# Performance work log

Hardware: AMD Instinct MI355X
Metric: run time of the kernel (lower is better)

## Reference

```python
import jax, jax.numpy as jnp
import numpy as np

TAU = 0.02  # softmax temperature (logits are divided by tau)


def setup_inputs() -> dict:
    key = jax.random.key(0)
    k1, k2 = jax.random.split(key)
    B, N, H, W = 4, 256, 256, 256
    H_img, W_img = 512, 512
    logits = jax.random.normal(k1, (B, N, H, W), dtype=jnp.float32)
    # ground-truth match coordinates (x, y) in image-pixel space
    gt_xy = jax.random.uniform(k2, (B, N, 2), dtype=jnp.float32) * jnp.array(
        [W_img - 1, H_img - 1], dtype=jnp.float32
    )
    # grid buffer: (H*W, 2) rows of (x, y), x fastest (meshgrid ij, stacked [xs, ys])
    ys, xs = jnp.meshgrid(jnp.arange(H), jnp.arange(W), indexing="ij")
    grid = jnp.stack([xs, ys], axis=-1).reshape(-1, 2).astype(jnp.float32)
    return {"logits": logits, "gt_xy": gt_xy, "grid": grid, "H_img": H_img, "W_img": W_img}


def reference(logits, gt_xy, grid, H_img, W_img):
    B, N, H, W = logits.shape
    # scale gt coords from image pixels to feature-map pixels (per-axis (new-1)/(old-1))
    scale_in = jnp.array([(W - 1) / (W_img - 1), (H - 1) / (H_img - 1)], dtype=logits.dtype)
    gt_fm = gt_xy * scale_in  # (B, N, 2)
    # temperature softmax over flattened spatial dim
    prob = jax.nn.softmax(logits.reshape(B, N, H * W) / TAU, axis=-1)  # (B, N, HW)
    # soft-argmax: expected (x, y) coordinate
    pred = jnp.einsum("bnl,lc->bnc", prob, grid)  # (B, N, 2)
    norm_scale = jnp.array([W - 1, H - 1], dtype=pred.dtype)
    pred_norm = 2.0 * pred / norm_scale - 1.0
    gt_norm = 2.0 * gt_fm / norm_scale - 1.0
    err = jnp.linalg.norm(pred_norm - gt_norm, axis=-1)  # (B, N)
    return err.sum()
```

## Files before the change

kernel.cpp:

```cpp
#include <hip/hip_runtime.h>
#include <math.h>

#define TAU_INV 50.0f

__device__ __forceinline__ void osm_merge(float& m, float& s, float& sx, float& sy,
                                          float m2, float s2, float sx2, float sy2) {
    float nm = fmaxf(m, m2);
    float c1 = __expf(m - nm);
    float c2 = __expf(m2 - nm);
    s  = s  * c1 + s2  * c2;
    sx = sx * c1 + sx2 * c2;
    sy = sy * c1 + sy2 * c2;
    m  = nm;
}

__device__ __forceinline__ void osm_elem(float& m, float& s, float& sx, float& sy,
                                         float a, float fx, float fy) {
    float nm = fmaxf(m, a);
    float c  = __expf(m - nm);
    float w  = __expf(a - nm);
    s  = fmaf(s,  c, w);
    sx = fmaf(sx, c, w * fx);
    sy = fmaf(sy, c, w * fy);
    m  = nm;
}

__global__ __launch_bounds__(256) void soft_argmax_part(
        const float* __restrict__ logits,
        float4* __restrict__ part,
        int W, int elems_per_blk, float invW) {
    const int blk = blockIdx.x;
    const int tid = threadIdx.x;
    const int nvec = elems_per_blk >> 2;
    const float4* b4 = (const float4*)logits + (size_t)blk * (size_t)nvec;
    const int base_l = (blk & 1) * elems_per_blk;

    float m = -INFINITY, s = 0.f, sx = 0.f, sy = 0.f;

    for (int i = tid; i < nvec; i += 512) {
        const int i1 = i + 256;
        float4 v0 = b4[i];
        float4 v1;
        bool have1 = (i1 < nvec);
        if (have1) v1 = b4[i1];

        {
            int l0 = base_l + (i << 2);
            int y0 = (int)((float)l0 * invW);
            if (y0 * W > l0) --y0;
            else if ((y0 + 1) * W <= l0) ++y0;
            int x0 = l0 - y0 * W;
            float fy = (float)y0;
            osm_elem(m, s, sx, sy, v0.x * TAU_INV, (float)(x0 + 0), fy);
            osm_elem(m, s, sx, sy, v0.y * TAU_INV, (float)(x0 + 1), fy);
            osm_elem(m, s, sx, sy, v0.z * TAU_INV, (float)(x0 + 2), fy);
            osm_elem(m, s, sx, sy, v0.w * TAU_INV, (float)(x0 + 3), fy);
        }
        if (have1) {
            int l0 = base_l + (i1 << 2);
            int y0 = (int)((float)l0 * invW);
            if (y0 * W > l0) --y0;
            else if ((y0 + 1) * W <= l0) ++y0;
            int x0 = l0 - y0 * W;
            float fy = (float)y0;
            osm_elem(m, s, sx, sy, v1.x * TAU_INV, (float)(x0 + 0), fy);
            osm_elem(m, s, sx, sy, v1.y * TAU_INV, (float)(x0 + 1), fy);
            osm_elem(m, s, sx, sy, v1.z * TAU_INV, (float)(x0 + 2), fy);
            osm_elem(m, s, sx, sy, v1.w * TAU_INV, (float)(x0 + 3), fy);
        }
    }

    #pragma unroll
    for (int off = 32; off >= 1; off >>= 1) {
        float m2  = __shfl_xor(m,  off);
        float s2  = __shfl_xor(s,  off);
        float sx2 = __shfl_xor(sx, off);
        float sy2 = __shfl_xor(sy, off);
        osm_merge(m, s, sx, sy, m2, s2, sx2, sy2);
    }

    __shared__ float sm[4], ss[4], ssx[4], ssy[4];
    const int wave = tid >> 6, lane = tid & 63;
    if (lane == 0) { sm[wave] = m; ss[wave] = s; ssx[wave] = sx; ssy[wave] = sy; }
    __syncthreads();

    if (tid == 0) {
        #pragma unroll
        for (int wv = 1; wv < 4; ++wv)
            osm_merge(m, s, sx, sy, sm[wv], ss[wv], ssx[wv], ssy[wv]);
        part[blk] = make_float4(m, s, sx, sy);
    }
}

__global__ __launch_bounds__(256) void finish(
        const float4* __restrict__ part,
        const float* __restrict__ gt_xy,
        const int* __restrict__ HimgP,
        const int* __restrict__ WimgP,
        float* __restrict__ out,
        int W, int H, int BN) {
    const int tid = threadIdx.x;
    const float Wimg = (float)WimgP[0];
    const float Himg = (float)HimgP[0];
    const float sxin = (float)(W - 1) / (Wimg - 1.f);
    const float syin = (float)(H - 1) / (Himg - 1.f);
    const float nx = 2.f / (float)(W - 1);
    const float ny = 2.f / (float)(H - 1);

    float acc = 0.f;
    for (int r = tid; r < BN; r += 256) {
        float4 p0 = part[2 * r + 0];
        float4 p1 = part[2 * r + 1];
        float m = p0.x, s = p0.y, sx = p0.z, sy = p0.w;
        osm_merge(m, s, sx, sy, p1.x, p1.y, p1.z, p1.w);
        float px = sx / s;
        float py = sy / s;
        float gx = gt_xy[2 * r + 0] * sxin;
        float gy = gt_xy[2 * r + 1] * syin;
        float dx = (px - gx) * nx;
        float dy = (py - gy) * ny;
        acc += sqrtf(dx * dx + dy * dy);
    }
    #pragma unroll
    for (int off = 32; off >= 1; off >>= 1) acc += __shfl_xor(acc, off);
    __shared__ float sw[4];
    const int wave = tid >> 6, lane = tid & 63;
    if (lane == 0) sw[wave] = acc;
    __syncthreads();
    if (tid == 0) out[0] = sw[0] + sw[1] + sw[2] + sw[3];
}

extern "C" void kernel_launch(void* const* d_in, const int* in_sizes, int n_in,
                              void* d_out, int out_size, void* d_ws, size_t ws_size,
                              hipStream_t stream) {
    const float* logits = (const float*)d_in[0];
    const float* gt_xy  = (const float*)d_in[1];
    const int*   HimgP  = (const int*)d_in[3];
    const int*   WimgP  = (const int*)d_in[4];

    const int HW = in_sizes[2] / 2;
    const int BN = in_sizes[1] / 2;
    int W = 1;
    while (W * W < HW) W <<= 1;
    if (W * W != HW) W = (int)(sqrtf((float)HW) + 0.5f);
    const int H = HW / W;

    float4* part = (float4*)d_ws;
    float*  out  = (float*)d_out;

    const int elems_per_blk = HW / 2;
    soft_argmax_part<<<2 * BN, 256, 0, stream>>>(logits, part, W, elems_per_blk,
                                                 1.0f / (float)W);
    finish<<<1, 256, 0, stream>>>(part, gt_xy, HimgP, WimgP, out, W, H, BN);
}
```

Measured before the change: 51.90 us.

## Fuse finish into soft-argmax kernel, vectorize online softmax per float4 with exp2

The separate finish kernel is folded into the main kernel through a last-block-done atomic counter, which removes one kernel launch. The per-element online softmax now works per float4: it takes a local max of four values, does four exp2 calls plus one merge, and computes x/y coordinates with shifts and masks. The inner loop is unrolled to four float4 loads per iteration to raise memory-level parallelism. The counter lives in the workspace, is never reset, and relies on modulo of gridDim. W is also assumed to be a power of two, and the non-square fallback was removed.

Result: slower. 105.3 us (+102.9%).

```diff
diff --git a/kernel.cpp b/kernel.cpp
--- a/kernel.cpp
+++ b/kernel.cpp
@@ -2,132 +2,142 @@
 #include <math.h>
 
 #define TAU_INV 50.0f
+#define LOG2E   1.4426950408889634f
 
-__device__ __forceinline__ void osm_merge(float& m, float& s, float& sx, float& sy,
-                                          float m2, float s2, float sx2, float sy2) {
-    float nm = fmaxf(m, m2);
-    float c1 = __expf(m - nm);
-    float c2 = __expf(m2 - nm);
-    s  = s  * c1 + s2  * c2;
-    sx = sx * c1 + sx2 * c2;
-    sy = sy * c1 + sy2 * c2;
-    m  = nm;
+#if __has_builtin(__builtin_amdgcn_exp2f)
+#define EXP2(x) __builtin_amdgcn_exp2f(x)
+#else
+#define EXP2(x) __expf((x) * 0.6931471805599453f)
+#endif
+
+struct Quad { float m, s, sx, sy; };
+
+__device__ __forceinline__ Quad qmerge(const Quad a, const Quad b) {
+    Quad r;
+    r.m = fmaxf(a.m, b.m);
+    float ca = EXP2(a.m - r.m);
+    float cb = EXP2(b.m - r.m);
+    r.s  = fmaf(a.s,  ca, b.s  * cb);
+    r.sx = fmaf(a.sx, ca, b.sx * cb);
+    r.sy = fmaf(a.sy, ca, b.sy * cb);
+    return r;
 }
 
-__device__ __forceinline__ void osm_elem(float& m, float& s, float& sx, float& sy,
-                                         float a, float fx, float fy) {
-    float nm = fmaxf(m, a);
-    float c  = __expf(m - nm);
-    float w  = __expf(a - nm);
-    s  = fmaf(s,  c, w);
-    sx = fmaf(sx, c, w * fx);
-    sy = fmaf(sy, c, w * fy);
-    m  = nm;
+__device__ __forceinline__ Quad quad_of(const float4 v, const float x0, const float fy) {
+    const float k = TAU_INV * LOG2E;
+    float a0 = v.x * k, a1 = v.y * k, a2 = v.z * k, a3 = v.w * k;
+    float m4 = fmaxf(fmaxf(a0, a1), fmaxf(a2, a3));
+    float w0 = EXP2(a0 - m4), w1 = EXP2(a1 - m4), w2 = EXP2(a2 - m4), w3 = EXP2(a3 - m4);
+    float ws = (w0 + w1) + (w2 + w3);
+    float wj = fmaf(3.f, w3, fmaf(2.f, w2, w1));
+    Quad q;
+    q.m  = m4;
+    q.s  = ws;
+    q.sx = fmaf(x0, ws, wj);
+    q.sy = fy * ws;
+    return q;
 }
 
-__global__ __launch_bounds__(256) void soft_argmax_part(
+__global__ __launch_bounds__(256) void soft_argmax_fused(
         const float* __restrict__ logits,
+        const float* __restrict__ gt_xy,
+        const int* __restrict__ HimgP,
+        const int* __restrict__ WimgP,
         float4* __restrict__ part,
-        int W, int elems_per_blk, float invW) {
+        unsigned* __restrict__ counter,
+        float* __restrict__ out,
+        int wshift, int elems_per_blk, int H, int BN) {
+    const int W = 1 << wshift;
+    const int wmask = W - 1;
     const int blk = blockIdx.x;
     const int tid = threadIdx.x;
     const int nvec = elems_per_blk >> 2;
-    const float4* b4 = (const float4*)logits + (size_t)blk * (size_t)nvec;
+    const float4* p = (const float4*)logits + (size_t)blk * (size_t)nvec;
     const int base_l = (blk & 1) * elems_per_blk;
 
-    float m = -INFINITY, s = 0.f, sx = 0.f, sy = 0.f;
+    Quad acc; acc.m = -INFINITY; acc.s = 0.f; acc.sx = 0.f; acc.sy = 0.f;
 
-    for (int i = tid; i < nvec; i += 512) {
-        const int i1 = i + 256;
-        float4 v0 = b4[i];
-        float4 v1;
-        bool have1 = (i1 < nvec);
-        if (have1) v1 = b4[i1];
-
-        {
-            int l0 = base_l + (i << 2);
-            int y0 = (int)((float)l0 * invW);
-            if (y0 * W > l0) --y0;
-            else if ((y0 + 1) * W <= l0) ++y0;
-            int x0 = l0 - y0 * W;
-            float fy = (float)y0;
-            osm_elem(m, s, sx, sy, v0.x * TAU_INV, (float)(x0 + 0), fy);
-            osm_elem(m, s, sx, sy, v0.y * TAU_INV, (float)(x0 + 1), fy);
-            osm_elem(m, s, sx, sy, v0.z * TAU_INV, (float)(x0 + 2), fy);
-            osm_elem(m, s, sx, sy, v0.w * TAU_INV, (float)(x0 + 3), fy);
-        }
-        if (have1) {
-            int l0 = base_l + (i1 << 2);
-            int y0 = (int)((float)l0 * invW);
-            if (y0 * W > l0) --y0;
-            else if ((y0 + 1) * W <= l0) ++y0;
-            int x0 = l0 - y0 * W;
-            float fy = (float)y0;
-            osm_elem(m, s, sx, sy, v1.x * TAU_INV, (float)(x0 + 0), fy);
-            osm_elem(m, s, sx, sy, v1.y * TAU_INV, (float)(x0 + 1), fy);
-            osm_elem(m, s, sx, sy, v1.z * TAU_INV, (float)(x0 + 2), fy);
-            osm_elem(m, s, sx, sy, v1.w * TAU_INV, (float)(x0 + 3), fy);
-        }
+    const int nfull = nvec & ~1023;
+    for (int i = tid; i < nfull; i += 1024) {
+        float4 v0 = p[i];
+        float4 v1 = p[i + 256];
+        float4 v2 = p[i + 512];
+        float4 v3 = p[i + 768];
+        int l0 = base_l + (i << 2);
+        int l1 = l0 + 1024, l2 = l0 + 2048, l3 = l0 + 3072;
+        Quad q0 = quad_of(v0, (float)(l0 & wmask), (float)(l0 >> wshift));
+        Quad q1 = quad_of(v1, (float)(l1 & wmask), (float)(l1 >> wshift));
+        Quad q2 = quad_of(v2, (float)(l2 & wmask), (float)(l2 >> wshift));
+        Quad q3 = quad_of(v3, (float)(l3 & wmask), (float)(l3 >> wshift));
+        acc = qmerge(acc, qmerge(qmerge(q0, q1), qmerge(q2, q3)));
+    }
+    for (int i = nfull + tid; i < nvec; i += 256) {
+        float4 v = p[i];
+        int l = base_l + (i << 2);
+        acc = qmerge(acc, quad_of(v, (float)(l & wmask), (float)(l >> wshift)));
     }
 
     #pragma unroll
     for (int off = 32; off >= 1; off >>= 1) {
-        float m2  = __shfl_xor(m,  off);
-        float s2  = __shfl_xor(s,  off);
-        float sx2 = __shfl_xor(sx, off);
-        float sy2 = __shfl_xor(sy, off);
-        osm_merge(m, s, sx, sy, m2, s2, sx2, sy2);
+        Quad o;
+        o.m  = __shfl_xor(acc.m,  off);
+        o.s  = __shfl_xor(acc.s,  off);
+        o.sx = __shfl_xor(acc.sx, off);
+        o.sy = __shfl_xor(acc.sy, off);
+        acc = qmerge(acc, o);
     }
 
-    __shared__ float sm[4], ss[4], ssx[4], ssy[4];
+    __shared__ float4 wq[4];
+    __shared__ int islast;
     const int wave = tid >> 6, lane = tid & 63;
-    if (lane == 0) { sm[wave] = m; ss[wave] = s; ssx[wave] = sx; ssy[wave] = sy; }
+    if (lane == 0) wq[wave] = make_float4(acc.m, acc.s, acc.sx, acc.sy);
     __syncthreads();
 
     if (tid == 0) {
         #pragma unroll
-        for (int wv = 1; wv < 4; ++wv)
-            osm_merge(m, s, sx, sy, sm[wv], ss[wv], ssx[wv], ssy[wv]);
-        part[blk] = make_float4(m, s, sx, sy);
+        for (int wv = 1; wv < 4; ++wv) {
+            float4 t = wq[wv];
+            Quad o; o.m = t.x; o.s = t.y; o.sx = t.z; o.sy = t.w;
+            acc = qmerge(acc, o);
+        }
+        part[blk] = make_float4(acc.m, acc.s, acc.sx, acc.sy);
+        __threadfence();
+        unsigned old = atomicAdd(counter, 1u);
+        unsigned g = (unsigned)gridDim.x;
+        islast = ((old % g) == g - 1u) ? 1 : 0;
     }
-}
+    __syncthreads();
 
-__global__ __launch_bounds__(256) void finish(
-        const float4* __restrict__ part,
-        const float* __restrict__ gt_xy,
-        const int* __restrict__ HimgP,
-        const int* __restrict__ WimgP,
-        float* __restrict__ out,
-        int W, int H, int BN) {
-    const int tid = threadIdx.x;
-    const float Wimg = (float)WimgP[0];
-    const float Himg = (float)HimgP[0];
-    const float sxin = (float)(W - 1) / (Wimg - 1.f);
-    const float syin = (float)(H - 1) / (Himg - 1.f);
-    const float nx = 2.f / (float)(W - 1);
-    const float ny = 2.f / (float)(H - 1);
-
-    float acc = 0.f;
-    for (int r = tid; r < BN; r += 256) {
-        float4 p0 = part[2 * r + 0];
-        float4 p1 = part[2 * r + 1];
-        float m = p0.x, s = p0.y, sx = p0.z, sy = p0.w;
-        osm_merge(m, s, sx, sy, p1.x, p1.y, p1.z, p1.w);
-        float px = sx / s;
-        float py = sy / s;
-        float gx = gt_xy[2 * r + 0] * sxin;
-        float gy = gt_xy[2 * r + 1] * syin;
-        float dx = (px - gx) * nx;
-        float dy = (py - gy) * ny;
-        acc += sqrtf(dx * dx + dy * dy);
+    if (islast) {
+        __threadfence();
+        const float Wimg = (float)WimgP[0];
+        const float Himg = (float)HimgP[0];
+        const float sxin = (float)(W - 1) / (Wimg - 1.f);
+        const float syin = (float)(H - 1) / (Himg - 1.f);
+        const float nx = 2.f / (float)(W - 1);
+        const float ny = 2.f / (float)(H - 1);
+        float accE = 0.f;
+        for (int r = tid; r < BN; r += 256) {
+            float4 p0 = part[2 * r + 0];
+            float4 p1 = part[2 * r + 1];
+            Quad a; a.m = p0.x; a.s = p0.y; a.sx = p0.z; a.sy = p0.w;
+            Quad b; b.m = p1.x; b.s = p1.y; b.sx = p1.z; b.sy = p1.w;
+            Quad t = qmerge(a, b);
+            float px = t.sx / t.s;
+            float py = t.sy / t.s;
+            float gx = gt_xy[2 * r + 0] * sxin;
+            float gy = gt_xy[2 * r + 1] * syin;
+            float dx = (px - gx) * nx;
+            float dy = (py - gy) * ny;
+            accE += sqrtf(dx * dx + dy * dy);
+        }
+        #pragma unroll
+        for (int off = 32; off >= 1; off >>= 1) accE += __shfl_xor(accE, off);
+        __shared__ float sw[4];
+        if (lane == 0) sw[wave] = accE;
+        __syncthreads();
+        if (tid == 0) out[0] = sw[0] + sw[1] + sw[2] + sw[3];
     }
-    #pragma unroll
-    for (int off = 32; off >= 1; off >>= 1) acc += __shfl_xor(acc, off);
-    __shared__ float sw[4];
-    const int wave = tid >> 6, lane = tid & 63;
-    if (lane == 0) sw[wave] = acc;
-    __syncthreads();
-    if (tid == 0) out[0] = sw[0] + sw[1] + sw[2] + sw[3];
 }
 
 extern "C" void kernel_launch(void* const* d_in, const int* in_sizes, int n_in,
@@ -142,14 +152,16 @@
     const int BN = in_sizes[1] / 2;
     int W = 1;
     while (W * W < HW) W <<= 1;
-    if (W * W != HW) W = (int)(sqrtf((float)HW) + 0.5f);
     const int H = HW / W;
+    int wshift = 0;
+    while ((1 << wshift) < W) ++wshift;
 
-    float4* part = (float4*)d_ws;
-    float*  out  = (float*)d_out;
+    float4*   part    = (float4*)d_ws;
+    unsigned* counter = (unsigned*)((char*)d_ws + (size_t)2 * BN * sizeof(float4));
+    float*    out     = (float*)d_out;
 
     const int elems_per_blk = HW / 2;
-    soft_argmax_part<<<2 * BN, 256, 0, stream>>>(logits, part, W, elems_per_blk,
-                                                 1.0f / (float)W);
-    finish<<<1, 256, 0, stream>>>(part, gt_xy, HimgP, WimgP, out, W, H, BN);
+    soft_argmax_fused<<<2 * BN, 256, 0, stream>>>(
+        logits, gt_xy, HimgP, WimgP, part, counter, out,
+        wshift, elems_per_blk, H, BN);
 }
```
